# Kernel optimization log

Hardware: AMD Instinct MI355X
Metric: run time of the kernel (lower is better)

Reference implementation:

```python
import jax, jax.numpy as jnp
import numpy as np
import math

BS, SEQ = 2048, 50
REL, ETYPE = 6, 4
ATT, HEADS, HEAD = 64, 4, 16
HID, OUT = 128, 64


def setup_inputs() -> dict:
    key = jax.random.key(0)
    ks = jax.random.split(key, 20)
    d = {}
    d['input_seqs'] = jax.random.normal(ks[0], (BS, SEQ, 3, 3, REL), jnp.float32)
    d['input_edge_types'] = jax.random.uniform(ks[1], (BS, SEQ, 3, 3, ETYPE), jnp.float32)
    d['input_masks'] = jax.random.randint(ks[2], (BS, SEQ, 3, 3), 0, 2, jnp.int32)
    def lin(k, fin, fout):
        k1, k2 = jax.random.split(k)
        bound = 1.0 / math.sqrt(fin)
        W = jax.random.uniform(k1, (fout, fin), jnp.float32, -bound, bound)
        b = jax.random.uniform(k2, (fout,), jnp.float32, -bound, bound)
        return W, b
    d['W_fus'], d['b_fus'] = lin(ks[3], REL + ETYPE + 9, 64)
    d['Wk'], d['bk'] = lin(ks[4], REL, ATT)
    d['Wq'], d['bq'] = lin(ks[5], 64, ATT)
    d['Wv'], d['bv'] = lin(ks[6], 64, ATT)
    bound = 1.0 / math.sqrt(HID)
    d['W_ih'] = jax.random.uniform(ks[7], (4 * HID, ATT), jnp.float32, -bound, bound)
    d['W_hh'] = jax.random.uniform(ks[8], (4 * HID, HID), jnp.float32, -bound, bound)
    d['b_ih'] = jax.random.uniform(ks[9], (4 * HID,), jnp.float32, -bound, bound)
    d['b_hh'] = jax.random.uniform(ks[10], (4 * HID,), jnp.float32, -bound, bound)
    d['W_out'], d['b_out'] = lin(ks[11], HID, OUT)
    return d


def _lstm_last(xs, W_ih, W_hh, b_ih, b_hh):
    # xs: (seq, bs, ATT); torch LSTM gate order i,f,g,o. Returns last hidden state.
    b = b_ih + b_hh
    def step(carry, x):
        h, c = carry
        gates = x @ W_ih.T + h @ W_hh.T + b
        i, f, g, o = jnp.split(gates, 4, axis=-1)
        i, f, o = jax.nn.sigmoid(i), jax.nn.sigmoid(f), jax.nn.sigmoid(o)
        g = jnp.tanh(g)
        c = f * c + i * g
        h = o * jnp.tanh(c)
        return (h, c), None
    h0 = jnp.zeros((xs.shape[1], HID), xs.dtype)
    (h, _), _ = jax.lax.scan(step, (h0, h0), xs)
    return h


def reference(input_seqs, input_edge_types, input_masks, W_fus, b_fus, Wk, bk, Wq, bq, Wv, bv, W_ih, W_hh, b_ih, b_hh, W_out, b_out):
    bs, seq = input_seqs.shape[0], input_seqs.shape[1]
    # location one-hot for the 3x3 neighborhood
    loc = jnp.broadcast_to(jnp.eye(9, dtype=input_seqs.dtype).reshape(3, 3, 9), (bs, seq, 3, 3, 9))
    edge_info = jnp.concatenate([input_seqs, input_edge_types, loc], axis=-1)
    edge_info = edge_info @ W_fus.T + b_fus                 # (bs, seq, 3, 3, 64)
    edge_info = edge_info.reshape(bs, seq, 9, 64)
    self_info = input_seqs[:, :, 1, 1]                       # (bs, seq, REL)
    # key from self state (same for all 9 slots), query/value from edge info
    key = (self_info @ Wk.T + bk).reshape(bs, seq, 1, HEADS, HEAD)     # broadcast over 9
    query = (edge_info @ Wq.T + bq).reshape(bs, seq, 9, HEADS, HEAD)
    value = (edge_info @ Wv.T + bv).reshape(bs, seq, 9, HEADS, HEAD)
    # att: dot over head dim -> (bs, seq, heads, 9)
    att = jnp.einsum('bsnhd,bsnhd->bshn', jnp.broadcast_to(key, query.shape), query) / math.sqrt(HEAD)
    mask9 = input_masks.reshape(bs, seq, 1, 9)               # broadcast over heads
    att = jnp.where(mask9 == 0, jnp.float32(-1e10), att)
    att = jax.nn.softmax(att, axis=-1)                       # (bs, seq, heads, 9)
    ctx = jnp.einsum('bshn,bsnhd->bshd', att, value)         # (bs, seq, heads, head)
    ctx = ctx.reshape(bs, seq, ATT).transpose(1, 0, 2)       # (seq, bs, ATT)
    h_last = _lstm_last(ctx, W_ih, W_hh, b_ih, b_hh)         # (bs, HID)
    return h_last @ W_out.T + b_out                          # (bs, OUT)
```

## Files before the change

### kernel.cpp

```cpp
#include <hip/hip_runtime.h>
#include <math.h>

#define BS   2048
#define SEQ  50
#define NPOS (BS * SEQ)

typedef __attribute__((ext_vector_type(8))) short bf16x8;
typedef __attribute__((ext_vector_type(4))) float f32x4;

__device__ __forceinline__ float sigf(float x) { return 1.0f / (1.0f + __expf(-x)); }
__device__ __forceinline__ float tanhfast(float x) {
    float e = __expf(2.0f * x);
    return 1.0f - 2.0f / (e + 1.0f);
}
__device__ __forceinline__ unsigned short bfrn(float x) {
    unsigned int u = __float_as_uint(x);
    u += 0x7FFFu + ((u >> 16) & 1u);
    return (unsigned short)(u >> 16);
}
__device__ __forceinline__ float bf2f(unsigned short h) {
    return __uint_as_float(((unsigned int)h) << 16);
}

#define FMA4(A, X, W) \
    A = fmaf((X).x, (W).x, A); A = fmaf((X).y, (W).y, A); \
    A = fmaf((X).z, (W).z, A); A = fmaf((X).w, (W).w, A);

__device__ float Wvf_d[640];
__device__ float Ce_d[576];
__device__ float Ag_d[280];
__device__ float Bd_d[252];

__global__ __launch_bounds__(512) void prep_all(
    const float* __restrict__ Wih, const float* __restrict__ Whh,
    bf16x8* __restrict__ whF, bf16x8* __restrict__ wiF,
    const float* __restrict__ Wf, const float* __restrict__ bf,
    const float* __restrict__ Wq, const float* __restrict__ bq,
    const float* __restrict__ Wv,
    const float* __restrict__ Wk, const float* __restrict__ bk)
{
    __shared__ float sG[640];
    __shared__ float sD[576];

    if (blockIdx.x < 48) {
        int id = blockIdx.x * 512 + threadIdx.x;
        const float* src;
        bf16x8* dst;
        int p;
        if (id < 16384) {
            int l = id & 63, frag = id >> 6;
            p = frag & 1;
            int kc = (frag >> 1) & 3, ti = (frag >> 3) & 3, w = frag >> 5;
            int n  = (w + 8 * ti) * 16 + (l & 15);
            int k0 = kc * 32 + (l >> 4) * 8;
            src = &Whh[n * 128 + k0];
            dst = &whF[frag * 64 + l];
        } else {
            int id2 = id - 16384;
            int l = id2 & 63, frag = id2 >> 6;
            p = frag & 1;
            int kc = (frag >> 1) & 1, tile = frag >> 2;
            int n  = tile * 16 + (l & 15);
            int k0 = kc * 32 + (l >> 4) * 8;
            src = &Wih[n * 64 + k0];
            dst = &wiF[frag * 64 + l];
        }
        bf16x8 v;
        #pragma unroll
        for (int j = 0; j < 8; ++j) {
            float x = src[j];
            unsigned short hi = bfrn(x);
            unsigned short r  = p ? bfrn(x - bf2f(hi)) : hi;
            v[j] = (short)r;
        }
        *dst = v;
        return;
    }

    if (blockIdx.x < 51) {
        int i = (blockIdx.x - 48) * 512 + threadIdx.x;
        if (i >= 1216) return;
        if (i < 640) {
            int o = i / 10, k = i % 10;
            float s = 0.f;
            #pragma unroll 8
            for (int j = 0; j < 64; ++j) s = fmaf(Wv[o * 64 + j], Wf[j * 19 + k], s);
            Wvf_d[i] = s;
        } else {
            int i2 = i - 640;
            int o = i2 / 9, e = i2 % 9;
            float s = 0.f;
            #pragma unroll 8
            for (int j = 0; j < 64; ++j)
                s = fmaf(Wf[j * 19 + 10 + e] + bf[j], Wv[o * 64 + j], s);
            Ce_d[i2] = s;
        }
        return;
    }

    const int t = threadIdx.x;
    for (int i = t; i < 1216; i += 512) {
        if (i < 640) {
            int n = i / 10, k = i % 10;
            float s = 0.f;
            #pragma unroll 8
            for (int j = 0; j < 64; ++j) s = fmaf(Wq[n * 64 + j], Wf[j * 19 + k], s);
            sG[i] = s;
        } else {
            int i2 = i - 640;
            int e = i2 >> 6, n = i2 & 63;
            float s = bq[n];
            #pragma unroll 8
            for (int j = 0; j < 64; ++j)
                s = fmaf(Wf[j * 19 + 10 + e] + bf[j], Wq[n * 64 + j], s);
            sD[i2] = s;
        }
    }
    __syncthreads();
    for (int i = t; i < 532; i += 512) {
        if (i < 280) {
            int h = i / 70, rem = i % 70, k = rem / 7, jj = rem % 7;
            float s = 0.f;
            #pragma unroll
            for (int d = 0; d < 16; ++d) {
                int n = h * 16 + d;
                float wkj = (jj < 6) ? Wk[n * 6 + jj] : bk[n];
                s = fmaf(wkj, sG[n * 10 + k], s);
            }
            Ag_d[i] = s;
        } else {
            int i4 = i - 280;
            int e = i4 / 28, rem = i4 % 28, h = rem / 7, jj = rem % 7;
            float s = 0.f;
            #pragma unroll
            for (int d = 0; d < 16; ++d) {
                int n = h * 16 + d;
                float wkj = (jj < 6) ? Wk[n * 6 + jj] : bk[n];
                s = fmaf(wkj, sD[e * 64 + n], s);
            }
            Bd_d[i4] = s;
        }
    }
}

__global__ __launch_bounds__(256) void edge_attn_ctx(
    const float* __restrict__ seqs,
    const float* __restrict__ ets,
    const int*   __restrict__ masks,
    const float* __restrict__ bv,
    float* __restrict__ ctx)
{
    const int p = blockIdx.x * 256 + threadIdx.x;
    if (p >= NPOS) return;
    const float* sp = seqs + p * 54;
    const float* ep = ets  + p * 36;
    const int*   mp = masks + p * 9;

    const float s0 = sp[24], s1 = sp[25], s2 = sp[26],
                s3 = sp[27], s4 = sp[28], s5 = sp[29];

    float g[4][10];
    #pragma unroll
    for (int h = 0; h < 4; ++h)
        #pragma unroll
        for (int k = 0; k < 10; ++k) {
            const float* a = &Ag_d[(h * 10 + k) * 7];
            float v = a[6];
            v = fmaf(s0, a[0], v); v = fmaf(s1, a[1], v);
            v = fmaf(s2, a[2], v); v = fmaf(s3, a[3], v);
            v = fmaf(s4, a[4], v); v = fmaf(s5, a[5], v);
            g[h][k] = v;
        }

    float att[9][4];
    float mx0 = -3.0e38f, mx1 = -3.0e38f, mx2 = -3.0e38f, mx3 = -3.0e38f;
    #pragma unroll
    for (int e = 0; e < 9; ++e) {
        float r0 = sp[e*6+0], r1 = sp[e*6+1], r2 = sp[e*6+2],
              r3 = sp[e*6+3], r4 = sp[e*6+4], r5 = sp[e*6+5];
        float r6 = ep[e*4+0], r7 = ep[e*4+1], r8 = ep[e*4+2], r9 = ep[e*4+3];
        const int mk = mp[e];
        #pragma unroll
        for (int h = 0; h < 4; ++h) {
            const float* b = &Bd_d[(e * 4 + h) * 7];
            float a = b[6];
            a = fmaf(s0, b[0], a); a = fmaf(s1, b[1], a);
            a = fmaf(s2, b[2], a); a = fmaf(s3, b[3], a);
            a = fmaf(s4, b[4], a); a = fmaf(s5, b[5], a);
            a = fmaf(r0, g[h][0], a); a = fmaf(r1, g[h][1], a);
            a = fmaf(r2, g[h][2], a); a = fmaf(r3, g[h][3], a);
            a = fmaf(r4, g[h][4], a); a = fmaf(r5, g[h][5], a);
            a = fmaf(r6, g[h][6], a); a = fmaf(r7, g[h][7], a);
            a = fmaf(r8, g[h][8], a); a = fmaf(r9, g[h][9], a);
            a *= 0.25f;
            a = (mk == 0) ? -1.0e10f : a;
            att[e][h] = a;
            if (h == 0) mx0 = fmaxf(mx0, a);
            if (h == 1) mx1 = fmaxf(mx1, a);
            if (h == 2) mx2 = fmaxf(mx2, a);
            if (h == 3) mx3 = fmaxf(mx3, a);
        }
    }

    float ss0 = 0.f, ss1 = 0.f, ss2 = 0.f, ss3 = 0.f;
    #pragma unroll
    for (int e = 0; e < 9; ++e) {
        att[e][0] = __expf(att[e][0] - mx0); ss0 += att[e][0];
        att[e][1] = __expf(att[e][1] - mx1); ss1 += att[e][1];
        att[e][2] = __expf(att[e][2] - mx2); ss2 += att[e][2];
        att[e][3] = __expf(att[e][3] - mx3); ss3 += att[e][3];
    }

    float rb[4][10];
    #pragma unroll
    for (int h = 0; h < 4; ++h)
        #pragma unroll
        for (int k = 0; k < 10; ++k) rb[h][k] = 0.f;
    #pragma unroll
    for (int e = 0; e < 9; ++e) {
        float r0 = sp[e*6+0], r1 = sp[e*6+1], r2 = sp[e*6+2],
              r3 = sp[e*6+3], r4 = sp[e*6+4], r5 = sp[e*6+5];
        float r6 = ep[e*4+0], r7 = ep[e*4+1], r8 = ep[e*4+2], r9 = ep[e*4+3];
        #pragma unroll
        for (int h = 0; h < 4; ++h) {
            const float w = att[e][h];
            rb[h][0] = fmaf(w, r0, rb[h][0]); rb[h][1] = fmaf(w, r1, rb[h][1]);
            rb[h][2] = fmaf(w, r2, rb[h][2]); rb[h][3] = fmaf(w, r3, rb[h][3]);
            rb[h][4] = fmaf(w, r4, rb[h][4]); rb[h][5] = fmaf(w, r5, rb[h][5]);
            rb[h][6] = fmaf(w, r6, rb[h][6]); rb[h][7] = fmaf(w, r7, rb[h][7]);
            rb[h][8] = fmaf(w, r8, rb[h][8]); rb[h][9] = fmaf(w, r9, rb[h][9]);
        }
    }
    const float iv0 = 1.f / ss0, iv1 = 1.f / ss1, iv2 = 1.f / ss2, iv3 = 1.f / ss3;

    float* cp = ctx + p * 64;
    #pragma unroll
    for (int o = 0; o < 64; ++o) {
        const int h = o >> 4;
        const float inv = (h == 0) ? iv0 : (h == 1) ? iv1 : (h == 2) ? iv2 : iv3;
        const float* wv = &Wvf_d[o * 10];
        const float* ce = &Ce_d[o * 9];
        float acc = 0.f;
        #pragma unroll
        for (int k = 0; k < 10; ++k) acc = fmaf(rb[h][k], wv[k], acc);
        #pragma unroll
        for (int e = 0; e < 9; ++e) acc = fmaf(att[e][h], ce[e], acc);
        cp[o] = acc * inv + bv[o];
    }
}

#define MFMA16(A, B, C) __builtin_amdgcn_mfma_f32_16x16x32_bf16(A, B, C, 0, 0, 0)
#define MM4(F, W0, W1, W2, W3) \
    a0 = MFMA16(F, W0, a0); a1 = MFMA16(F, W1, a1); \
    a2 = MFMA16(F, W2, a2); a3 = MFMA16(F, W3, a3);

#define HPASS \
    MM4(hfh[0], whr[0][0][0], whr[1][0][0], whr[2][0][0], whr[3][0][0]) \
    MM4(hfh[1], whr[0][1][0], whr[1][1][0], whr[2][1][0], whr[3][1][0]) \
    MM4(hfh[2], whr[0][2][0], whr[1][2][0], whr[2][2][0], whr[3][2][0]) \
    MM4(hfh[3], whr[0][3][0], whr[1][3][0], whr[2][3][0], whr[3][3][0]) \
    MM4(hfl[0], whr[0][0][0], whr[1][0][0], whr[2][0][0], whr[3][0][0]) \
    MM4(hfl[1], whr[0][1][0], whr[1][1][0], whr[2][1][0], whr[3][1][0]) \
    MM4(hfl[2], whr[0][2][0], whr[1][2][0], whr[2][2][0], whr[3][2][0]) \
    MM4(hfl[3], whr[0][3][0], whr[1][3][0], whr[2][3][0], whr[3][3][0]) \
    MM4(hfh[0], whr[0][0][1], whr[1][0][1], whr[2][0][1], whr[3][0][1]) \
    MM4(hfh[1], whr[0][1][1], whr[1][1][1], whr[2][1][1], whr[3][1][1]) \
    MM4(hfh[2], whr[0][2][1], whr[1][2][1], whr[2][2][1], whr[3][2][1]) \
    MM4(hfh[3], whr[0][3][1], whr[1][3][1], whr[2][3][1], whr[3][3][1])

#define REDIST_E(ch, g0, g1) { \
    float s2_ = __shfl_xor(ch[2], 32), s3_ = __shfl_xor(ch[3], 32); \
    g0 = lolq ? ch[0] : s2_;  g1 = lolq ? ch[1] : s3_; }
#define REDIST_O(ch, g0, g1) { \
    float s0_ = __shfl_xor(ch[0], 32), s1_ = __shfl_xor(ch[1], 32); \
    g0 = lolq ? s0_ : ch[2];  g1 = lolq ? s1_ : ch[3]; }

#define PWBODY(gi0,gf0,gg0,go0,gi1,gf1,gg1,go1, WB0, WB1) { \
    float i0_ = sigf(gi0 + bi), f0_ = sigf(gf0 + bff); \
    float gA_ = tanhfast(gg0 + bg), o0_ = sigf(go0 + bo); \
    c20 = fmaf(f0_, c20, i0_ * gA_); \
    float hv0_ = o0_ * tanhfast(c20); \
    float i1_ = sigf(gi1 + bi), f1_ = sigf(gf1 + bff); \
    float gB_ = tanhfast(gg1 + bg), o1_ = sigf(go1 + bo); \
    c21 = fmaf(f1_, c21, i1_ * gB_); \
    float hv1_ = o1_ * tanhfast(c21); \
    unsigned short hh0_ = bfrn(hv0_), hh1_ = bfrn(hv1_); \
    unsigned short hl0_ = bfrn(hv0_ - bf2f(hh0_)), hl1_ = bfrn(hv1_ - bf2f(hh1_)); \
    *(unsigned short*)((char*)s_hh + (WB0)) = hh0_; \
    *(unsigned short*)((char*)s_hl + (WB0)) = hl0_; \
    *(unsigned short*)((char*)s_hh + (WB1)) = hh1_; \
    *(unsigned short*)((char*)s_hl + (WB1)) = hl1_; }

__global__ __launch_bounds__(512, 2) void lstm_mfma(
    const float*  __restrict__ ctx,
    const bf16x8* __restrict__ whF,
    const bf16x8* __restrict__ wiFg,
    const float*  __restrict__ b_ih, const float* __restrict__ b_hh,
    const float*  __restrict__ W_out, const float* __restrict__ b_out,
    float* __restrict__ out)
{
    const int t  = threadIdx.x;
    const int w  = t >> 6, l = t & 63;
    const int lm = l & 15, lq = l >> 4;
    const int row0 = blockIdx.x * 8;

    __shared__ unsigned short s_xh[1024], s_xl[1024];
    __shared__ unsigned short s_hh[4096], s_hl[4096];

    for (int i = t; i < 1024; i += 512) { s_xh[i] = 0; s_xl[i] = 0; }
    for (int i = t; i < 4096; i += 512) { s_hh[i] = 0; s_hl[i] = 0; }

    bf16x8 whr[4][4][2];
    #pragma unroll
    for (int ti = 0; ti < 4; ++ti)
        #pragma unroll
        for (int kc = 0; kc < 4; ++kc)
            #pragma unroll
            for (int p = 0; p < 2; ++p)
                whr[ti][kc][p] = whF[(((w * 4 + ti) * 4 + kc) * 2 + p) * 64 + l];

    bf16x8 wir[2][4][2];
    #pragma unroll
    for (int kc = 0; kc < 2; ++kc)
        #pragma unroll
        for (int ti = 0; ti < 4; ++ti)
            #pragma unroll
            for (int p = 0; p < 2; ++p)
                wir[kc][ti][p] = wiFg[(((w + 8 * ti) * 2 + kc) * 2 + p) * 64 + l];

    const int m = w * 16 + lm;
    const float bi  = b_ih[m]       + b_hh[m];
    const float bff = b_ih[128 + m] + b_hh[128 + m];
    const float bg  = b_ih[256 + m] + b_hh[256 + m];
    const float bo  = b_ih[384 + m] + b_hh[384 + m];

    const int  urb  = ((lq & 1) << 2) | (lq & 2);
    const bool lolq = (lq < 2);
    float c20 = 0.f, c21 = 0.f;

    const int xrow  = t >> 5;
    const int xl32  = t & 31;
    const int srow  = xrow & 7;
    const int spair = xrow >> 3;
    const float2* ctx2 = (const float2*)ctx;
    const int xbase = (row0 + srow) * SEQ + spair;
    const int xwb   = xrow * 128 + ((4 * xl32) ^ ((xrow & 7) << 4));
    const int swzr  = (lm & 7) << 4;
    const int hwb_m = 32 * w + 2 * lm;
    const int wb0e = 4096 + (8 + urb) * 256 + (hwb_m ^ (urb << 4));
    const int wb1e = 4096 + (9 + urb) * 256 + (hwb_m ^ ((urb + 1) << 4));
    const int wb0o = urb * 256 + (hwb_m ^ (urb << 4));
    const int wb1o = (urb + 1) * 256 + (hwb_m ^ ((urb + 1) << 4));

    float2 xv = ctx2[xbase * 32 + xl32];

    for (int u = 0; u < SEQ / 2; ++u) {
        {
            unsigned short xh0 = bfrn(xv.x), xh1 = bfrn(xv.y);
            unsigned short xl0 = bfrn(xv.x - bf2f(xh0)), xl1 = bfrn(xv.y - bf2f(xh1));
            *(unsigned int*)((char*)s_xh + xwb) = (unsigned int)xh0 | ((unsigned int)xh1 << 16);
            *(unsigned int*)((char*)s_xl + xwb) = (unsigned int)xl0 | ((unsigned int)xl1 << 16);
        }
        __syncthreads();

        float2 xvn = make_float2(0.f, 0.f);
        if (u + 1 < SEQ / 2) xvn = ctx2[(xbase + 2 * u + 2) * 32 + xl32];

        bf16x8 hfh[4], hfl[4];
        if (u > 0) {
            #pragma unroll
            for (int kc = 0; kc < 4; ++kc) {
                int b = lm * 256 + ((kc * 64 + lq * 16) ^ swzr);
                hfh[kc] = *(const bf16x8*)((const char*)s_hh + b);
                hfl[kc] = *(const bf16x8*)((const char*)s_hl + b);
            }
        }
        bf16x8 xfh[2], xfl[2];
        #pragma unroll
        for (int kc = 0; kc < 2; ++kc) {
            int b = lm * 128 + ((kc * 64 + lq * 16) ^ swzr);
            xfh[kc] = *(const bf16x8*)((const char*)s_xh + b);
            xfl[kc] = *(const bf16x8*)((const char*)s_xl + b);
        }

        f32x4 a0 = {0.f,0.f,0.f,0.f}, a1 = a0, a2 = a0, a3 = a0;

        if (u > 0) { HPASS }

        #pragma unroll
        for (int kc = 0; kc < 2; ++kc) {
            MM4(xfh[kc], wir[kc][0][0], wir[kc][1][0], wir[kc][2][0], wir[kc][3][0])
            MM4(xfl[kc], wir[kc][0][0], wir[kc][1][0], wir[kc][2][0], wir[kc][3][0])
            MM4(xfh[kc], wir[kc][0][1], wir[kc][1][1], wir[kc][2][1], wir[kc][3][1])
        }

        {
            float gi0, gi1, gf0, gf1, gg0, gg1, go0, go1;
            REDIST_E(a0, gi0, gi1)
            REDIST_E(a1, gf0, gf1)
            REDIST_E(a2, gg0, gg1)
            REDIST_E(a3, go0, go1)
            PWBODY(gi0, gf0, gg0, go0, gi1, gf1, gg1, go1, wb0e, wb1e)
        }

        __syncthreads();
        #pragma unroll
        for (int kc = 0; kc < 4; ++kc) {
            int b = 4096 + lm * 256 + ((kc * 64 + lq * 16) ^ swzr);
            hfh[kc] = *(const bf16x8*)((const char*)s_hh + b);
            hfl[kc] = *(const bf16x8*)((const char*)s_hl + b);
        }
        HPASS

        {
            float gi0, gi1, gf0, gf1, gg0, gg1, go0, go1;
            REDIST_O(a0, gi0, gi1)
            REDIST_O(a1, gf0, gf1)
            REDIST_O(a2, gg0, gg1)
            REDIST_O(a3, go0, go1)
            PWBODY(gi0, gf0, gg0, go0, gi1, gf1, gg1, go1, wb0o, wb1o)
        }
        xv = xvn;
    }
    __syncthreads();

    {
        const int row = t >> 5;
        if (row < 8) {
            const int j0 = t & 31, j1 = (t & 31) + 32;
            const int rswz = (row & 7) << 4;
            float accA = b_out[j0], accB = b_out[j1];
            #pragma unroll
            for (int kq = 0; kq < 16; ++kq) {
                int b = row * 256 + ((kq * 16) ^ rswz);
                bf16x8 hh8 = *(const bf16x8*)((const char*)s_hh + b);
                bf16x8 hl8 = *(const bf16x8*)((const char*)s_hl + b);
                #pragma unroll
                for (int e = 0; e < 8; ++e) {
                    float h = bf2f((unsigned short)hh8[e]) + bf2f((unsigned short)hl8[e]);
                    int k = kq * 8 + e;
                    accA = fmaf(h, W_out[j0 * 128 + k], accA);
                    accB = fmaf(h, W_out[j1 * 128 + k], accB);
                }
            }
            out[(row0 + row) * 64 + j0] = accA;
            out[(row0 + row) * 64 + j1] = accB;
        }
    }
}

extern "C" void kernel_launch(void* const* d_in, const int* in_sizes, int n_in,
                              void* d_out, int out_size, void* d_ws, size_t ws_size,
                              hipStream_t stream) {
    (void)in_sizes; (void)n_in; (void)out_size; (void)ws_size;
    const float* seqs  = (const float*)d_in[0];
    const float* ets   = (const float*)d_in[1];
    const int*   masks = (const int*)d_in[2];
    const float* Wf  = (const float*)d_in[3];
    const float* bf  = (const float*)d_in[4];
    const float* Wk  = (const float*)d_in[5];
    const float* bk  = (const float*)d_in[6];
    const float* Wq  = (const float*)d_in[7];
    const float* bq  = (const float*)d_in[8];
    const float* Wv  = (const float*)d_in[9];
    const float* bv  = (const float*)d_in[10];
    const float* Wih = (const float*)d_in[11];
    const float* Whh = (const float*)d_in[12];
    const float* bih = (const float*)d_in[13];
    const float* bhh = (const float*)d_in[14];
    const float* Wo  = (const float*)d_in[15];
    const float* bo  = (const float*)d_in[16];

    char* ws = (char*)d_ws;
    bf16x8* whF = (bf16x8*)(ws);
    bf16x8* wiF = (bf16x8*)(ws + 262144);
    float*  ctx = (float*) (ws + 262144 + 131072);

    hipLaunchKernelGGL(prep_all, dim3(52), dim3(512), 0, stream,
                       Wih, Whh, whF, wiF, Wf, bf, Wq, bq, Wv, Wk, bk);
    hipLaunchKernelGGL(edge_attn_ctx, dim3(400), dim3(256), 0, stream,
                       seqs, ets, masks, bv, ctx);
    hipLaunchKernelGGL(lstm_mfma, dim3(256), dim3(512), 0, stream,
                       ctx, whF, wiF, bih, bhh, Wo, bo, (float*)d_out);
}
```

Measured before the change: 246.0 us.

## Split edge attention across heads with one wavefront per head and online softmax

The edge attention kernel now gives each of the four heads its own wavefront, so one position is handled by four threads instead of one, and the grid grows to match. Each thread computes a single-pass online softmax with a running max and rescaled accumulators, and loads inputs with float2/float4 vectors. Each thread writes its 16 context outputs as float4 stores. This lowers per-thread register pressure and serial work to raise parallelism, but every head re-reads the same per-position inputs and does a few extra exponentials for the online rescaling.

New measurement: 234.8 us. 4.5% less time.

```diff
diff --git a/kernel.cpp b/kernel.cpp
--- a/kernel.cpp
+++ b/kernel.cpp
@@ -150,102 +150,102 @@
     const float* __restrict__ bv,
     float* __restrict__ ctx)
 {
-    const int p = blockIdx.x * 256 + threadIdx.x;
-    if (p >= NPOS) return;
-    const float* sp = seqs + p * 54;
-    const float* ep = ets  + p * 36;
-    const int*   mp = masks + p * 9;
-
-    const float s0 = sp[24], s1 = sp[25], s2 = sp[26],
-                s3 = sp[27], s4 = sp[28], s5 = sp[29];
-
-    float g[4][10];
-    #pragma unroll
-    for (int h = 0; h < 4; ++h)
-        #pragma unroll
-        for (int k = 0; k < 10; ++k) {
-            const float* a = &Ag_d[(h * 10 + k) * 7];
-            float v = a[6];
-            v = fmaf(s0, a[0], v); v = fmaf(s1, a[1], v);
-            v = fmaf(s2, a[2], v); v = fmaf(s3, a[3], v);
-            v = fmaf(s4, a[4], v); v = fmaf(s5, a[5], v);
-            g[h][k] = v;
-        }
-
-    float att[9][4];
-    float mx0 = -3.0e38f, mx1 = -3.0e38f, mx2 = -3.0e38f, mx3 = -3.0e38f;
+    const int lane = threadIdx.x & 63;
+    const int hu   = __builtin_amdgcn_readfirstlane(threadIdx.x >> 6);
+    const int p    = blockIdx.x * 64 + lane;
+
+    const float* sp = seqs  + (size_t)p * 54;
+    const float* ep = ets   + (size_t)p * 36;
+    const int*   mp = masks + (size_t)p * 9;
+
+    float2 sA = *(const float2*)(sp + 24);
+    float2 sB = *(const float2*)(sp + 26);
+    float2 sC = *(const float2*)(sp + 28);
+    const float s0 = sA.x, s1 = sA.y, s2 = sB.x,
+                s3 = sB.y, s4 = sC.x, s5 = sC.y;
+
+    float g[10];
+    #pragma unroll
+    for (int k = 0; k < 10; ++k) {
+        const float* a = &Ag_d[(hu * 10 + k) * 7];
+        float v = a[6];
+        v = fmaf(s0, a[0], v); v = fmaf(s1, a[1], v);
+        v = fmaf(s2, a[2], v); v = fmaf(s3, a[3], v);
+        v = fmaf(s4, a[4], v); v = fmaf(s5, a[5], v);
+        g[k] = v;
+    }
+
+    float att[9], rb[10];
+    #pragma unroll
+    for (int k = 0; k < 10; ++k) rb[k] = 0.f;
+    float m = -3.0e38f, s = 0.f;
     #pragma unroll
     for (int e = 0; e < 9; ++e) {
-        float r0 = sp[e*6+0], r1 = sp[e*6+1], r2 = sp[e*6+2],
-              r3 = sp[e*6+3], r4 = sp[e*6+4], r5 = sp[e*6+5];
-        float r6 = ep[e*4+0], r7 = ep[e*4+1], r8 = ep[e*4+2], r9 = ep[e*4+3];
+        float2 r01 = *(const float2*)(sp + e * 6);
+        float2 r23 = *(const float2*)(sp + e * 6 + 2);
+        float2 r45 = *(const float2*)(sp + e * 6 + 4);
+        float4 r69 = *(const float4*)(ep + e * 4);
         const int mk = mp[e];
-        #pragma unroll
-        for (int h = 0; h < 4; ++h) {
-            const float* b = &Bd_d[(e * 4 + h) * 7];
-            float a = b[6];
-            a = fmaf(s0, b[0], a); a = fmaf(s1, b[1], a);
-            a = fmaf(s2, b[2], a); a = fmaf(s3, b[3], a);
-            a = fmaf(s4, b[4], a); a = fmaf(s5, b[5], a);
-            a = fmaf(r0, g[h][0], a); a = fmaf(r1, g[h][1], a);
-            a = fmaf(r2, g[h][2], a); a = fmaf(r3, g[h][3], a);
-            a = fmaf(r4, g[h][4], a); a = fmaf(r5, g[h][5], a);
-            a = fmaf(r6, g[h][6], a); a = fmaf(r7, g[h][7], a);
-            a = fmaf(r8, g[h][8], a); a = fmaf(r9, g[h][9], a);
-            a *= 0.25f;
-            a = (mk == 0) ? -1.0e10f : a;
-            att[e][h] = a;
-            if (h == 0) mx0 = fmaxf(mx0, a);
-            if (h == 1) mx1 = fmaxf(mx1, a);
-            if (h == 2) mx2 = fmaxf(mx2, a);
-            if (h == 3) mx3 = fmaxf(mx3, a);
-        }
-    }
-
-    float ss0 = 0.f, ss1 = 0.f, ss2 = 0.f, ss3 = 0.f;
-    #pragma unroll
-    for (int e = 0; e < 9; ++e) {
-        att[e][0] = __expf(att[e][0] - mx0); ss0 += att[e][0];
-        att[e][1] = __expf(att[e][1] - mx1); ss1 += att[e][1];
-        att[e][2] = __expf(att[e][2] - mx2); ss2 += att[e][2];
-        att[e][3] = __expf(att[e][3] - mx3); ss3 += att[e][3];
-    }
-
-    float rb[4][10];
-    #pragma unroll
-    for (int h = 0; h < 4; ++h)
-        #pragma unroll
-        for (int k = 0; k < 10; ++k) rb[h][k] = 0.f;
-    #pragma unroll
-    for (int e = 0; e < 9; ++e) {
-        float r0 = sp[e*6+0], r1 = sp[e*6+1], r2 = sp[e*6+2],
-              r3 = sp[e*6+3], r4 = sp[e*6+4], r5 = sp[e*6+5];
-        float r6 = ep[e*4+0], r7 = ep[e*4+1], r8 = ep[e*4+2], r9 = ep[e*4+3];
-        #pragma unroll
-        for (int h = 0; h < 4; ++h) {
-            const float w = att[e][h];
-            rb[h][0] = fmaf(w, r0, rb[h][0]); rb[h][1] = fmaf(w, r1, rb[h][1]);
-            rb[h][2] = fmaf(w, r2, rb[h][2]); rb[h][3] = fmaf(w, r3, rb[h][3]);
-            rb[h][4] = fmaf(w, r4, rb[h][4]); rb[h][5] = fmaf(w, r5, rb[h][5]);
-            rb[h][6] = fmaf(w, r6, rb[h][6]); rb[h][7] = fmaf(w, r7, rb[h][7]);
-            rb[h][8] = fmaf(w, r8, rb[h][8]); rb[h][9] = fmaf(w, r9, rb[h][9]);
-        }
-    }
-    const float iv0 = 1.f / ss0, iv1 = 1.f / ss1, iv2 = 1.f / ss2, iv3 = 1.f / ss3;
-
-    float* cp = ctx + p * 64;
-    #pragma unroll
-    for (int o = 0; o < 64; ++o) {
-        const int h = o >> 4;
-        const float inv = (h == 0) ? iv0 : (h == 1) ? iv1 : (h == 2) ? iv2 : iv3;
-        const float* wv = &Wvf_d[o * 10];
-        const float* ce = &Ce_d[o * 9];
-        float acc = 0.f;
-        #pragma unroll
-        for (int k = 0; k < 10; ++k) acc = fmaf(rb[h][k], wv[k], acc);
-        #pragma unroll
-        for (int e = 0; e < 9; ++e) acc = fmaf(att[e][h], ce[e], acc);
-        cp[o] = acc * inv + bv[o];
+
+        const float* b = &Bd_d[(e * 4 + hu) * 7];
+        float a = b[6];
+        a = fmaf(s0, b[0], a); a = fmaf(s1, b[1], a);
+        a = fmaf(s2, b[2], a); a = fmaf(s3, b[3], a);
+        a = fmaf(s4, b[4], a); a = fmaf(s5, b[5], a);
+        a = fmaf(r01.x, g[0], a); a = fmaf(r01.y, g[1], a);
+        a = fmaf(r23.x, g[2], a); a = fmaf(r23.y, g[3], a);
+        a = fmaf(r45.x, g[4], a); a = fmaf(r45.y, g[5], a);
+        a = fmaf(r69.x, g[6], a); a = fmaf(r69.y, g[7], a);
+        a = fmaf(r69.z, g[8], a); a = fmaf(r69.w, g[9], a);
+        a *= 0.25f;
+        a = (mk == 0) ? -1.0e10f : a;
+        att[e] = a;
+
+        float nm = fmaxf(m, a);
+        float sc = __expf(m - nm);
+        float w  = __expf(a - nm);
+        s = fmaf(s, sc, w);
+        rb[0] = fmaf(rb[0], sc, w * r01.x);
+        rb[1] = fmaf(rb[1], sc, w * r01.y);
+        rb[2] = fmaf(rb[2], sc, w * r23.x);
+        rb[3] = fmaf(rb[3], sc, w * r23.y);
+        rb[4] = fmaf(rb[4], sc, w * r45.x);
+        rb[5] = fmaf(rb[5], sc, w * r45.y);
+        rb[6] = fmaf(rb[6], sc, w * r69.x);
+        rb[7] = fmaf(rb[7], sc, w * r69.y);
+        rb[8] = fmaf(rb[8], sc, w * r69.z);
+        rb[9] = fmaf(rb[9], sc, w * r69.w);
+        m = nm;
+    }
+
+    const float inv = 1.f / s;
+    float we[9];
+    #pragma unroll
+    for (int e = 0; e < 9; ++e) we[e] = __expf(att[e] - m) * inv;
+    float rbn[10];
+    #pragma unroll
+    for (int k = 0; k < 10; ++k) rbn[k] = rb[k] * inv;
+
+    float4* cp = (float4*)(ctx + (size_t)p * 64 + hu * 16);
+    #pragma unroll
+    for (int i4 = 0; i4 < 4; ++i4) {
+        float r0_, r1_, r2_, r3_;
+        #pragma unroll
+        for (int j = 0; j < 4; ++j) {
+            const int o = hu * 16 + i4 * 4 + j;
+            const float* wv = &Wvf_d[o * 10];
+            const float* ce = &Ce_d[o * 9];
+            float acc = bv[o];
+            #pragma unroll
+            for (int k = 0; k < 10; ++k) acc = fmaf(rbn[k], wv[k], acc);
+            #pragma unroll
+            for (int e = 0; e < 9; ++e) acc = fmaf(we[e], ce[e], acc);
+            if (j == 0) r0_ = acc;
+            if (j == 1) r1_ = acc;
+            if (j == 2) r2_ = acc;
+            if (j == 3) r3_ = acc;
+        }
+        cp[i4] = make_float4(r0_, r1_, r2_, r3_);
     }
 }
 
@@ -478,7 +478,7 @@
 
     hipLaunchKernelGGL(prep_all, dim3(52), dim3(512), 0, stream,
                        Wih, Whh, whF, wiF, Wf, bf, Wq, bq, Wv, Wk, bk);
-    hipLaunchKernelGGL(edge_attn_ctx, dim3(400), dim3(256), 0, stream,
+    hipLaunchKernelGGL(edge_attn_ctx, dim3(1600), dim3(256), 0, stream,
                        seqs, ets, masks, bv, ctx);
     hipLaunchKernelGGL(lstm_mfma, dim3(256), dim3(512), 0, stream,
                        ctx, whF, wiF, bih, bhh, Wo, bo, (float*)d_out);
```
